# Kernel optimization log

Hardware: AMD Instinct MI355X
Metric: run time of the kernel (lower is better)

## Reference

```python
import jax, jax.numpy as jnp
import numpy as np
import math

B, N, D_IN, D_OUT = 8, 2048, 128, 128
NEG_BIG = -10000.0

def setup_inputs() -> dict:
    key = jax.random.key(0)
    k_in, k_adj, kq, kk, kv, kbq, kbk, kbv = jax.random.split(key, 8)
    scale = 1.0 / math.sqrt(D_IN)
    inputs = jax.random.normal(k_in, (B, N, D_IN), dtype=jnp.float32)
    adj = jax.random.randint(k_adj, (B, N, N), 0, 2, dtype=jnp.int32)
    Wq = jax.random.uniform(kq, (D_IN, D_OUT), jnp.float32, -scale, scale)
    Wk = jax.random.uniform(kk, (D_IN, D_OUT), jnp.float32, -scale, scale)
    Wv = jax.random.uniform(kv, (D_IN, D_OUT), jnp.float32, -scale, scale)
    bq = jax.random.uniform(kbq, (D_OUT,), jnp.float32, -scale, scale)
    bk = jax.random.uniform(kbk, (D_OUT,), jnp.float32, -scale, scale)
    bv = jax.random.uniform(kbv, (D_OUT,), jnp.float32, -scale, scale)
    return {"inputs": inputs, "adj": adj, "Wq": Wq, "bq": bq,
            "Wk": Wk, "bk": bk, "Wv": Wv, "bv": bv}

def reference(inputs, adj, Wq, bq, Wk, bk, Wv, bv):
    # QKV projections: [B, N, D_OUT]
    q = inputs @ Wq + bq
    k = inputs @ Wk + bk
    v = inputs @ Wv + bv
    # additive adjacency bias: 0 where edge, -10000 where no edge
    bias = (1.0 - adj.astype(jnp.float32)) * NEG_BIG
    # scaled dot-product scores [B, N, N]
    a = jnp.einsum('bnd,bmd->bnm', q, k) / jnp.sqrt(jnp.float32(q.shape[-1]))
    a = a + bias
    p = jax.nn.softmax(a, axis=-1)  # dropout_prob=0.0 -> identity
    h = jnp.einsum('bnm,bmd->bnd', p, v)
    return jax.nn.elu(h)
```

## Files before the change

kernel.cpp:

```cpp
#include <hip/hip_runtime.h>

typedef unsigned short u16;
typedef __bf16 bf16x8 __attribute__((ext_vector_type(8)));
typedef float  fx4    __attribute__((ext_vector_type(4)));

__device__ __forceinline__ u16 f2bf(float f) {
    unsigned int x = __builtin_bit_cast(unsigned int, f);
    x = x + 0x7fffu + ((x >> 16) & 1u);
    return (u16)(x >> 16);
}
__device__ __forceinline__ __bf16 f2bf16(float f) {
    return __builtin_bit_cast(__bf16, f2bf(f));
}
__device__ __forceinline__ u16 f2bf_fast(float f) {
    return __builtin_bit_cast(u16, (__bf16)f);
}
__device__ __forceinline__ float exp2_fast(float x) {
#if __has_builtin(__builtin_amdgcn_exp2f)
    return __builtin_amdgcn_exp2f(x);
#else
    float r;
    __asm__ volatile("v_exp_f32 %0, %1" : "=v"(r) : "v"(x));
    return r;
#endif
}

#define MFMA16(a, b, c) __builtin_amdgcn_mfma_f32_16x16x32_bf16((a), (b), (c), 0, 0, 0)
#define WAVE_LDS_SYNC() __asm__ volatile("s_waitcnt lgkmcnt(0)" ::: "memory")

__global__ __launch_bounds__(256) void wt_kernel(
    const float* __restrict__ Wq, const float* __restrict__ Wk,
    const float* __restrict__ Wv, u16* __restrict__ WT)
{
    const int o = blockIdx.x * 256 + threadIdx.x;
    const int p = o >> 14, rem = o & 16383, c = rem >> 7, k = rem & 127;
    const float* W = (p == 0) ? Wq : ((p == 1) ? Wk : Wv);
    WT[o] = f2bf(W[k * 128 + c]);
}

__global__ __launch_bounds__(256, 2) void qkv_kernel(
    const float* __restrict__ X, const u16* __restrict__ WT,
    const float* __restrict__ bq, const float* __restrict__ bk,
    const float* __restrict__ bv,
    u16* __restrict__ Qf, u16* __restrict__ Kf, u16* __restrict__ Vf)
{
    const int tid  = threadIdx.x;
    const int w    = tid >> 6;
    const int lane = tid & 63;
    const int n    = lane & 15;
    const int quad = lane >> 4;
    const int gw   = blockIdx.x * 4 + w;
    const int rt   = gw >> 1, ch = gw & 1;
    const int row0 = rt * 16;
    const int b    = row0 >> 11;
    const int keyb = row0 & 2047;

    bf16x8 af[4];
    {
        const float* xr = X + (size_t)(row0 + n) * 128;
#pragma unroll
        for (int kk = 0; kk < 4; ++kk) {
            float4 f0 = *(const float4*)(xr + kk * 32 + quad * 8);
            float4 f1 = *(const float4*)(xr + kk * 32 + quad * 8 + 4);
            bf16x8 a;
            a[0] = f2bf16(f0.x); a[1] = f2bf16(f0.y); a[2] = f2bf16(f0.z); a[3] = f2bf16(f0.w);
            a[4] = f2bf16(f1.x); a[5] = f2bf16(f1.y); a[6] = f2bf16(f1.z); a[7] = f2bf16(f1.w);
            af[kk] = a;
        }
    }

    const float* Bs[2] = {bq, bk};
#pragma unroll
    for (int p = 0; p < 2; ++p) {
        const u16* wt = WT + p * 16384;
#pragma unroll
        for (int nt = 0; nt < 4; ++nt) {
            const int col0 = ch * 64 + nt * 16;
            fx4 acc = {0.f, 0.f, 0.f, 0.f};
#pragma unroll
            for (int kk = 0; kk < 4; ++kk) {
                bf16x8 bf = __builtin_bit_cast(bf16x8,
                    *(const uint4*)&wt[(col0 + n) * 128 + kk * 32 + quad * 8]);
                acc = MFMA16(af[kk], bf, acc);
            }
            const float bb = Bs[p][col0 + n];
            const int c = col0 + n;
            const int kk_s = c >> 5, quad_s = (c >> 3) & 3, j = c & 7;
            u16* dst;
            if (p == 0) {
                dst = Qf + (((size_t)(b * 128 + (keyb >> 4)) * 4 + kk_s) << 9)
                         + quad_s * 128 + j;
            } else {
                dst = Kf + (((size_t)((b * 64 + (keyb >> 5)) * 2 + ((keyb >> 4) & 1)) * 4 + kk_s) << 9)
                         + quad_s * 128 + j;
            }
#pragma unroll
            for (int r = 0; r < 4; ++r)
                dst[(quad * 4 + r) * 8] = f2bf(acc[r] + bb);
        }
    }

    {
        const u16* wtv = WT + 2 * 16384;
        const int key = keyb + n;
        const int t = key >> 5, quad_v = (key >> 3) & 3, jv = key & 7;
#pragma unroll
        for (int d0 = 0; d0 < 4; ++d0) {
            const int dbase = ch * 64 + d0 * 16;
            fx4 acc = {0.f, 0.f, 0.f, 0.f};
#pragma unroll
            for (int kk = 0; kk < 4; ++kk) {
                bf16x8 wf = __builtin_bit_cast(bf16x8,
                    *(const uint4*)&wtv[(dbase + n) * 128 + kk * 32 + quad * 8]);
                acc = MFMA16(wf, af[kk], acc);
            }
            u16* dv = Vf + (((size_t)(b * 64 + t) * 8 + (dbase >> 4)) << 9)
                         + quad_v * 128 + jv;
#pragma unroll
            for (int r = 0; r < 4; ++r)
                dv[(quad * 4 + r) * 8] = f2bf(acc[r] + bv[dbase + quad * 4 + r]);
        }
    }
}

__global__ __launch_bounds__(256, 4) void attn_kernel(
    const u16* __restrict__ Qf, const u16* __restrict__ Kf,
    const u16* __restrict__ Vf, const int* __restrict__ adj,
    float* __restrict__ out)
{
    __shared__ __align__(16) float mO[4][16 * 128];
    __shared__ __align__(16) float ml[4][16];
    __shared__ __align__(16) u16 pl[4][640];

    const int tid  = threadIdx.x;
    const int h    = tid >> 6;
    const int lane = tid & 63;
    const int n    = lane & 15;
    const int quad = lane >> 4;
    const int b    = blockIdx.x & 7;
    const int qt   = blockIdx.x >> 3;
    const int q0   = qt * 16;
    const size_t bN = (size_t)b * 2048;

    bf16x8 qf[4];
    {
        const u16* qp = Qf + ((size_t)(b * 128 + qt) << 11) + lane * 8;
#pragma unroll
        for (int kk = 0; kk < 4; ++kk)
            qf[kk] = __builtin_bit_cast(bf16x8, *(const uint4*)(qp + (kk << 9)));
    }
    const u16* Kb = Kf + ((size_t)b << 18);
    const u16* Vb = Vf + ((size_t)b << 18);

    fx4 O[8];
#pragma unroll
    for (int i = 0; i < 8; ++i) O[i] = (fx4){0.f, 0.f, 0.f, 0.f};
    fx4 Lacc = {0.f, 0.f, 0.f, 0.f};

    bf16x8 ONESF;
    {
        const __bf16 one = __builtin_bit_cast(__bf16, (u16)0x3F80);
#pragma unroll
        for (int j = 0; j < 8; ++j) ONESF[j] = one;
    }

    const int* adjb = adj + (bN + q0 + quad * 4) * 2048;
    const float C2 = 0.12751742f;
    const float MB = -14427.0f;
    u16* pw = pl[h];

    float b0c[4], b1c[4];
    {
        const int k0 = h * 512;
#pragma unroll
        for (int r = 0; r < 4; ++r) {
            b0c[r] = adjb[(size_t)r * 2048 + k0 + n]      ? 0.f : MB;
            b1c[r] = adjb[(size_t)r * 2048 + k0 + 16 + n] ? 0.f : MB;
        }
    }

    for (int t = 0; t < 16; ++t) {
        const int tg = h * 16 + t;
        const u16* kt_ = Kb + ((size_t)tg << 12) + lane * 8;
        const u16* vt_ = Vb + ((size_t)tg << 12) + lane * 8;

        float b0n[4], b1n[4];
        if (t < 15) {
            const int kn = h * 512 + (t + 1) * 32;
#pragma unroll
            for (int r = 0; r < 4; ++r) {
                b0n[r] = adjb[(size_t)r * 2048 + kn + n]      ? 0.f : MB;
                b1n[r] = adjb[(size_t)r * 2048 + kn + 16 + n] ? 0.f : MB;
            }
        }

        fx4 S0 = {0.f, 0.f, 0.f, 0.f}, S1 = {0.f, 0.f, 0.f, 0.f};
#pragma unroll
        for (int kk = 0; kk < 4; ++kk) {
            bf16x8 kb0 = __builtin_bit_cast(bf16x8, *(const uint4*)(kt_ + (kk << 9)));
            bf16x8 kb1 = __builtin_bit_cast(bf16x8, *(const uint4*)(kt_ + ((4 + kk) << 9)));
            S0 = MFMA16(qf[kk], kb0, S0);
            S1 = MFMA16(qf[kk], kb1, S1);
        }

#pragma unroll
        for (int r = 0; r < 4; ++r) {
            const float e0 = exp2_fast(__builtin_fmaf(S0[r], C2, b0c[r]));
            const float e1 = exp2_fast(__builtin_fmaf(S1[r], C2, b1c[r]));
            pw[(quad * 4 + r) * 40 + n]      = f2bf_fast(e0);
            pw[(quad * 4 + r) * 40 + 16 + n] = f2bf_fast(e1);
        }

        WAVE_LDS_SYNC();
        bf16x8 pf = __builtin_bit_cast(bf16x8, *(const uint4*)&pw[n * 40 + quad * 8]);

#pragma unroll
        for (int dt = 0; dt < 8; ++dt) {
            bf16x8 vf = __builtin_bit_cast(bf16x8, *(const uint4*)(vt_ + (dt << 9)));
            O[dt] = MFMA16(pf, vf, O[dt]);
        }
        Lacc = MFMA16(pf, ONESF, Lacc);

#pragma unroll
        for (int r = 0; r < 4; ++r) { b0c[r] = b0n[r]; b1c[r] = b1n[r]; }
    }

#pragma unroll
    for (int r = 0; r < 4; ++r) {
        const int row = quad * 4 + r;
        if (n == 0) ml[h][row] = Lacc[r];
#pragma unroll
        for (int dt = 0; dt < 8; ++dt)
            mO[h][row * 128 + dt * 16 + n] = O[dt][r];
    }
    __syncthreads();

#pragma unroll
    for (int r = 0; r < 4; ++r) {
        const int row = quad * 4 + r;
        const float L = ml[0][row] + ml[1][row] + ml[2][row] + ml[3][row];
        const float linv = 1.f / L;
        float* po = out + (bN + q0 + row) * 128;
#pragma unroll
        for (int dti = 0; dti < 2; ++dti) {
            const int dt = h * 2 + dti;
            float o = 0.f;
#pragma unroll
            for (int g = 0; g < 4; ++g) o += mO[g][row * 128 + dt * 16 + n];
            const float hh = o * linv;
            po[dt * 16 + n] = (hh > 0.f) ? hh : (__expf(hh) - 1.f);
        }
    }
}

extern "C" void kernel_launch(void* const* d_in, const int* in_sizes, int n_in,
                              void* d_out, int out_size, void* d_ws, size_t ws_size,
                              hipStream_t stream) {
    (void)in_sizes; (void)n_in; (void)out_size; (void)ws_size;
    const float* X   = (const float*)d_in[0];
    const int*   adj = (const int*)d_in[1];
    const float* Wq  = (const float*)d_in[2];
    const float* bq  = (const float*)d_in[3];
    const float* Wk  = (const float*)d_in[4];
    const float* bk  = (const float*)d_in[5];
    const float* Wv  = (const float*)d_in[6];
    const float* bv  = (const float*)d_in[7];
    float* out = (float*)d_out;

    u16* WT  = (u16*)d_out;
    u16* Qf  = (u16*)d_ws;
    u16* Kf  = Qf + (size_t)16384 * 128;
    u16* Vf  = Kf + (size_t)16384 * 128;

    wt_kernel<<<192, 256, 0, stream>>>(Wq, Wk, Wv, WT);
    qkv_kernel<<<512, 256, 0, stream>>>(X, WT, bq, bk, bv, Qf, Kf, Vf);
    attn_kernel<<<1024, 256, 0, stream>>>(Qf, Kf, Vf, adj, out);
}
```

Baseline: 287.8 us.

## Stage adjacency tiles through LDS with nontemporal loads; coalesce QKV stores

The attention kernel now loads each 16x32 adjacency tile with 128-bit nontemporal loads, two tiles ahead. It stages the tiles in a double-buffered, XOR-swizzled LDS region that reuses the mO buffer, replacing scattered 4-byte gathers. K and V fragments for a tile are all loaded up front to overlap with compute. The QKV kernel writes outputs into per-wave LDS first and then stores coalesced 16-byte chunks instead of strided 2-byte scatters. Costs are more LDS traffic, more registers per wave, and a new syncthreads before mO is reused.

```diff
diff --git a/kernel.cpp b/kernel.cpp
--- a/kernel.cpp
+++ b/kernel.cpp
@@ -3,6 +3,7 @@
 typedef unsigned short u16;
 typedef __bf16 bf16x8 __attribute__((ext_vector_type(8)));
 typedef float  fx4    __attribute__((ext_vector_type(4)));
+typedef unsigned int u32x4 __attribute__((ext_vector_type(4)));
 
 __device__ __forceinline__ u16 f2bf(float f) {
     unsigned int x = __builtin_bit_cast(unsigned int, f);
@@ -24,6 +25,9 @@
     return r;
 #endif
 }
+__device__ __forceinline__ u32x4 ld_nt4(const int* p) {
+    return __builtin_nontemporal_load((const u32x4*)p);
+}
 
 #define MFMA16(a, b, c) __builtin_amdgcn_mfma_f32_16x16x32_bf16((a), (b), (c), 0, 0, 0)
 #define WAVE_LDS_SYNC() __asm__ volatile("s_waitcnt lgkmcnt(0)" ::: "memory")
@@ -44,6 +48,8 @@
     const float* __restrict__ bv,
     u16* __restrict__ Qf, u16* __restrict__ Kf, u16* __restrict__ Vf)
 {
+    __shared__ __align__(16) u16 st[4][1024];
+
     const int tid  = threadIdx.x;
     const int w    = tid >> 6;
     const int lane = tid & 63;
@@ -55,6 +61,8 @@
     const int b    = row0 >> 11;
     const int keyb = row0 & 2047;
 
+    u16* sw = st[w];
+
     bf16x8 af[4];
     {
         const float* xr = X + (size_t)(row0 + n) * 128;
@@ -85,25 +93,26 @@
             }
             const float bb = Bs[p][col0 + n];
             const int c = col0 + n;
-            const int kk_s = c >> 5, quad_s = (c >> 3) & 3, j = c & 7;
-            u16* dst;
-            if (p == 0) {
-                dst = Qf + (((size_t)(b * 128 + (keyb >> 4)) * 4 + kk_s) << 9)
-                         + quad_s * 128 + j;
-            } else {
-                dst = Kf + (((size_t)((b * 64 + (keyb >> 5)) * 2 + ((keyb >> 4) & 1)) * 4 + kk_s) << 9)
-                         + quad_s * 128 + j;
-            }
+            const int li = ((c >> 5) & 1) * 512 + ((c >> 3) & 3) * 128 + (c & 7);
 #pragma unroll
             for (int r = 0; r < 4; ++r)
-                dst[(quad * 4 + r) * 8] = f2bf(acc[r] + bb);
-        }
+                sw[li + (quad * 4 + r) * 8] = f2bf(acc[r] + bb);
+        }
+        WAVE_LDS_SYNC();
+        u16* gbase;
+        if (p == 0) {
+            gbase = Qf + (((size_t)(b * 128 + (keyb >> 4)) * 4 + 2 * ch) << 9);
+        } else {
+            gbase = Kf + (((size_t)((b * 64 + (keyb >> 5)) * 2 + ((keyb >> 4) & 1)) * 4 + 2 * ch) << 9);
+        }
+        *(uint4*)(gbase + lane * 8)       = *(const uint4*)(sw + lane * 8);
+        *(uint4*)(gbase + 512 + lane * 8) = *(const uint4*)(sw + 512 + lane * 8);
     }
 
     {
         const u16* wtv = WT + 2 * 16384;
-        const int key = keyb + n;
-        const int t = key >> 5, quad_v = (key >> 3) & 3, jv = key & 7;
+        const int hk    = (keyb >> 4) & 1;
+        const int vtile = keyb >> 5;
 #pragma unroll
         for (int d0 = 0; d0 < 4; ++d0) {
             const int dbase = ch * 64 + d0 * 16;
@@ -114,11 +123,19 @@
                     *(const uint4*)&wtv[(dbase + n) * 128 + kk * 32 + quad * 8]);
                 acc = MFMA16(wf, af[kk], acc);
             }
-            u16* dv = Vf + (((size_t)(b * 64 + t) * 8 + (dbase >> 4)) << 9)
-                         + quad_v * 128 + jv;
+            const int li = d0 * 256 + ((n >> 3) & 1) * 128 + (n & 7);
 #pragma unroll
             for (int r = 0; r < 4; ++r)
-                dv[(quad * 4 + r) * 8] = f2bf(acc[r] + bv[dbase + quad * 4 + r]);
+                sw[li + (quad * 4 + r) * 8] = f2bf(acc[r] + bv[dbase + quad * 4 + r]);
+        }
+        WAVE_LDS_SYNC();
+        const int l5 = lane >> 5, lo = lane & 31;
+#pragma unroll
+        for (int i = 0; i < 2; ++i) {
+            const int c2 = l5 + 2 * i;
+            u16* g = Vf + (((size_t)(b * 64 + vtile) * 8 + ch * 4 + c2) << 9)
+                        + hk * 256 + lo * 8;
+            *(uint4*)g = *(const uint4*)(sw + c2 * 256 + lo * 8);
         }
     }
 }
@@ -131,6 +148,8 @@
     __shared__ __align__(16) float mO[4][16 * 128];
     __shared__ __align__(16) float ml[4][16];
     __shared__ __align__(16) u16 pl[4][640];
+
+    int* adjst = (int*)&mO[0][0];
 
     const int tid  = threadIdx.x;
     const int h    = tid >> 6;
@@ -142,6 +161,11 @@
     const int q0   = qt * 16;
     const size_t bN = (size_t)b * 2048;
 
+    const int rr = lane >> 2;
+    const int c4 = (lane & 3) * 8;
+    const int sx = quad << 3;
+    const int* agl = adj + (((size_t)(bN + q0 + rr)) << 11) + h * 512 + c4;
+
     bf16x8 qf[4];
     {
         const u16* qp = Qf + ((size_t)(b * 128 + qt) << 11) + lane * 8;
@@ -164,66 +188,67 @@
         for (int j = 0; j < 8; ++j) ONESF[j] = one;
     }
 
-    const int* adjb = adj + (bN + q0 + quad * 4) * 2048;
     const float C2 = 0.12751742f;
     const float MB = -14427.0f;
     u16* pw = pl[h];
 
-    float b0c[4], b1c[4];
-    {
-        const int k0 = h * 512;
-#pragma unroll
-        for (int r = 0; r < 4; ++r) {
-            b0c[r] = adjb[(size_t)r * 2048 + k0 + n]      ? 0.f : MB;
-            b1c[r] = adjb[(size_t)r * 2048 + k0 + 16 + n] ? 0.f : MB;
-        }
-    }
-
-    for (int t = 0; t < 16; ++t) {
-        const int tg = h * 16 + t;
-        const u16* kt_ = Kb + ((size_t)tg << 12) + lane * 8;
-        const u16* vt_ = Vb + ((size_t)tg << 12) + lane * 8;
-
-        float b0n[4], b1n[4];
-        if (t < 15) {
-            const int kn = h * 512 + (t + 1) * 32;
-#pragma unroll
-            for (int r = 0; r < 4; ++r) {
-                b0n[r] = adjb[(size_t)r * 2048 + kn + n]      ? 0.f : MB;
-                b1n[r] = adjb[(size_t)r * 2048 + kn + 16 + n] ? 0.f : MB;
-            }
-        }
-
-        fx4 S0 = {0.f, 0.f, 0.f, 0.f}, S1 = {0.f, 0.f, 0.f, 0.f};
-#pragma unroll
-        for (int kk = 0; kk < 4; ++kk) {
-            bf16x8 kb0 = __builtin_bit_cast(bf16x8, *(const uint4*)(kt_ + (kk << 9)));
-            bf16x8 kb1 = __builtin_bit_cast(bf16x8, *(const uint4*)(kt_ + ((4 + kk) << 9)));
-            S0 = MFMA16(qf[kk], kb0, S0);
-            S1 = MFMA16(qf[kk], kb1, S1);
-        }
-
-#pragma unroll
-        for (int r = 0; r < 4; ++r) {
-            const float e0 = exp2_fast(__builtin_fmaf(S0[r], C2, b0c[r]));
-            const float e1 = exp2_fast(__builtin_fmaf(S1[r], C2, b1c[r]));
-            pw[(quad * 4 + r) * 40 + n]      = f2bf_fast(e0);
-            pw[(quad * 4 + r) * 40 + 16 + n] = f2bf_fast(e1);
-        }
-
-        WAVE_LDS_SYNC();
-        bf16x8 pf = __builtin_bit_cast(bf16x8, *(const uint4*)&pw[n * 40 + quad * 8]);
-
-#pragma unroll
-        for (int dt = 0; dt < 8; ++dt) {
-            bf16x8 vf = __builtin_bit_cast(bf16x8, *(const uint4*)(vt_ + (dt << 9)));
-            O[dt] = MFMA16(pf, vf, O[dt]);
-        }
-        Lacc = MFMA16(pf, ONESF, Lacc);
-
-#pragma unroll
-        for (int r = 0; r < 4; ++r) { b0c[r] = b0n[r]; b1c[r] = b1n[r]; }
-    }
+    u32x4 rA0, rA1, rB0, rB1;
+    rA0 = ld_nt4(agl + 0);  rA1 = ld_nt4(agl + 4);
+    rB0 = ld_nt4(agl + 32); rB1 = ld_nt4(agl + 36);
+    {
+        int* sw0 = adjst + h * 1024 + rr * 32 + (c4 ^ sx);
+        *(u32x4*)sw0       = rA0;
+        *((u32x4*)sw0 + 1) = rA1;
+    }
+
+#define TILE_BODY(T, RA0_, RA1_, RB0_, RB1_, DO_ISSUE, DO_WRITE)                    \
+  {                                                                                 \
+    const int tg = h * 16 + (T);                                                    \
+    const u16* kt_ = Kb + ((size_t)tg << 12) + lane * 8;                            \
+    const u16* vt_ = Vb + ((size_t)tg << 12) + lane * 8;                            \
+    bf16x8 kb[8]; bf16x8 vv[8];                                                     \
+    _Pragma("unroll") for (int kk = 0; kk < 8; ++kk)                                \
+      kb[kk] = __builtin_bit_cast(bf16x8, *(const uint4*)(kt_ + (kk << 9)));        \
+    _Pragma("unroll") for (int dt = 0; dt < 8; ++dt)                                \
+      vv[dt] = __builtin_bit_cast(bf16x8, *(const uint4*)(vt_ + (dt << 9)));        \
+    if (DO_ISSUE) {                                                                 \
+      RA0_ = ld_nt4(agl + ((T) + 2) * 32);                                          \
+      RA1_ = ld_nt4(agl + ((T) + 2) * 32 + 4);                                      \
+    }                                                                               \
+    fx4 S0 = {0.f, 0.f, 0.f, 0.f}, S1 = {0.f, 0.f, 0.f, 0.f};                       \
+    _Pragma("unroll") for (int kk = 0; kk < 4; ++kk) {                              \
+      S0 = MFMA16(qf[kk], kb[kk], S0);                                              \
+      S1 = MFMA16(qf[kk], kb[4 + kk], S1);                                          \
+    }                                                                               \
+    WAVE_LDS_SYNC();                                                                \
+    const int* sr = adjst + h * 1024 + ((T) & 1) * 512;                             \
+    _Pragma("unroll") for (int r = 0; r < 4; ++r) {                                 \
+      const int a0 = sr[(quad * 4 + r) * 32 + (n ^ sx)];                            \
+      const int a1 = sr[(quad * 4 + r) * 32 + ((16 + n) ^ sx)];                     \
+      const float e0 = exp2_fast(__builtin_fmaf(S0[r], C2, a0 ? 0.f : MB));         \
+      const float e1 = exp2_fast(__builtin_fmaf(S1[r], C2, a1 ? 0.f : MB));         \
+      pw[(quad * 4 + r) * 40 + n]      = f2bf_fast(e0);                             \
+      pw[(quad * 4 + r) * 40 + 16 + n] = f2bf_fast(e1);                             \
+    }                                                                               \
+    WAVE_LDS_SYNC();                                                                \
+    bf16x8 pf = __builtin_bit_cast(bf16x8, *(const uint4*)&pw[n * 40 + quad * 8]);  \
+    _Pragma("unroll") for (int dt = 0; dt < 8; ++dt)                                \
+      O[dt] = MFMA16(pf, vv[dt], O[dt]);                                            \
+    Lacc = MFMA16(pf, ONESF, Lacc);                                                 \
+    if (DO_WRITE) {                                                                 \
+      int* sw_ = adjst + h * 1024 + (((T) + 1) & 1) * 512 + rr * 32 + (c4 ^ sx);    \
+      *(u32x4*)sw_       = RB0_;                                                    \
+      *((u32x4*)sw_ + 1) = RB1_;                                                    \
+    }                                                                               \
+  }
+
+    for (int tt = 0; tt < 16; tt += 2) {
+        TILE_BODY(tt,     rA0, rA1, rB0, rB1, (tt < 14), 1);
+        TILE_BODY(tt + 1, rB0, rB1, rA0, rA1, (tt < 13), (tt < 14));
+    }
+#undef TILE_BODY
+
+    __syncthreads();
 
 #pragma unroll
     for (int r = 0; r < 4; ++r) {
```

Measured after the change: 369.4 us. 28.3% more time.
